# Performance work log

Measured on AMD Instinct MI355X. Metric: run time of the kernel, lower is better.

The kernel has to match this reference:

```python
import jax, jax.numpy as jnp
import numpy as np

B, S, HID = 1, 2048, 2048
N_HEADS = 16
HEAD_DIM = HID // N_HEADS  # 128
ROPE_THETA = 10000.0
NEG_INF = -1e9


def setup_inputs() -> dict:
    key = jax.random.key(0)
    ks = jax.random.split(key, 5)
    hidden_states = jax.random.normal(ks[0], (B, S, HID), dtype=jnp.float32)
    scale = 1.0 / np.sqrt(HID)
    Wq = jax.random.normal(ks[1], (HID, HID), dtype=jnp.float32) * scale
    Wk = jax.random.normal(ks[2], (HID, HID), dtype=jnp.float32) * scale
    Wv = jax.random.normal(ks[3], (HID, HID), dtype=jnp.float32) * scale
    Wo = jax.random.normal(ks[4], (HID, HID), dtype=jnp.float32) * scale
    # additive causal mask [B, 1, S, S]: 0 on/below diag, -1e9 above
    causal = jnp.tril(jnp.ones((S, S), dtype=bool))
    attention_mask = jnp.where(causal, 0.0, NEG_INF).astype(jnp.float32)[None, None]
    attention_mask = jnp.broadcast_to(attention_mask, (B, 1, S, S))
    position_ids = jnp.broadcast_to(jnp.arange(S, dtype=jnp.int64)[None, :], (B, S))
    return {"hidden_states": hidden_states, "Wq": Wq, "Wk": Wk, "Wv": Wv,
            "Wo": Wo, "attention_mask": attention_mask, "position_ids": position_ids}


def _rotate_half(x):
    x1, x2 = jnp.split(x, 2, axis=-1)
    return jnp.concatenate((-x2, x1), axis=-1)


def _rope_cos_sin(position_ids, head_dim, dtype):
    inv_freq = 1.0 / (ROPE_THETA ** (jnp.arange(0, head_dim, 2, dtype=jnp.float32) / head_dim))
    freqs = position_ids.astype(jnp.float32)[:, :, None] * inv_freq[None, None, :]  # [b, s, d/2]
    emb = jnp.concatenate((freqs, freqs), axis=-1)  # [b, s, d]
    # unsqueeze_dim=1 -> broadcast over heads
    return jnp.cos(emb).astype(dtype)[:, None], jnp.sin(emb).astype(dtype)[:, None]


def reference(hidden_states, Wq, Wk, Wv, Wo, attention_mask, position_ids):
    b, s, h = hidden_states.shape
    d = HEAD_DIM
    def proj(W):
        return (hidden_states @ W.T).reshape(b, s, N_HEADS, d).transpose(0, 2, 1, 3)  # [b,h,s,d]
    q, k, v = proj(Wq), proj(Wk), proj(Wv)
    cos, sin = _rope_cos_sin(position_ids, d, q.dtype)
    q = q * cos + _rotate_half(q) * sin
    k = k * cos + _rotate_half(k) * sin
    scores = jnp.einsum('bhqd,bhkd->bhqk', q, k) / jnp.sqrt(jnp.float32(d))
    scores = scores + attention_mask
    probs = jax.nn.softmax(scores.astype(jnp.float32), axis=-1).astype(q.dtype)
    attn = jnp.einsum('bhqk,bhkd->bhqd', probs, v)
    out = attn.transpose(0, 2, 1, 3).reshape(b, s, h)
    return out @ Wo.T
```

## Files before the change

kernel.cpp:

```cpp
#include <hip/hip_runtime.h>

typedef _Float16 half8 __attribute__((ext_vector_type(8)));
typedef _Float16 half4 __attribute__((ext_vector_type(4)));
typedef float floatx4 __attribute__((ext_vector_type(4)));
typedef float floatx16 __attribute__((ext_vector_type(16)));

#define GLDS(gp, lp) __builtin_amdgcn_global_load_lds( \
    (const __attribute__((address_space(1))) void*)(gp), \
    (__attribute__((address_space(3))) void*)(lp), 16, 0, 0)

__global__ void cvt_f2h5(const float* __restrict__ s0, const float* __restrict__ s1,
                         const float* __restrict__ s2, const float* __restrict__ s3,
                         const float* __restrict__ s4,
                         _Float16* __restrict__ d0, _Float16* __restrict__ d1,
                         _Float16* __restrict__ d2, _Float16* __restrict__ d3,
                         _Float16* __restrict__ d4, int n8) {
  int i = blockIdx.x * 256 + threadIdx.x;
  if (i >= n8) return;
  const float* s; _Float16* d;
  switch (blockIdx.y) {
    case 0: s = s0; d = d0; break;
    case 1: s = s1; d = d1; break;
    case 2: s = s2; d = d2; break;
    case 3: s = s3; d = d3; break;
    default: s = s4; d = d4; break;
  }
  const float4* s4p = (const float4*)s;
  float4 a = s4p[2 * i], b = s4p[2 * i + 1];
  half8 h;
  h[0] = (_Float16)a.x; h[1] = (_Float16)a.y; h[2] = (_Float16)a.z; h[3] = (_Float16)a.w;
  h[4] = (_Float16)b.x; h[5] = (_Float16)b.y; h[6] = (_Float16)b.z; h[7] = (_Float16)b.w;
  *(half8*)(d + 8 * (size_t)i) = h;
}

__global__ __launch_bounds__(256) void transpose_k(const _Float16* __restrict__ src,
                                                   _Float16* __restrict__ dst) {
  __shared__ _Float16 t[64][72];
  const int r0 = blockIdx.y * 64, c0 = blockIdx.x * 64;
  const int tr = threadIdx.x >> 3, tc = (threadIdx.x & 7) * 8;
  #pragma unroll
  for (int p = 0; p < 2; ++p) {
    half8 v = *(const half8*)(src + (size_t)(r0 + p * 32 + tr) * 2048 + c0 + tc);
    *(half8*)&t[p * 32 + tr][tc] = v;
  }
  __syncthreads();
  #pragma unroll
  for (int p = 0; p < 2; ++p) {
    half8 v;
    #pragma unroll
    for (int j = 0; j < 8; ++j) v[j] = t[tc + j][p * 32 + tr];
    *(half8*)(dst + (size_t)(c0 + p * 32 + tr) * 2048 + r0 + tc) = v;
  }
}

template <int OUTF, int BN>
__global__ __launch_bounds__(256) void gemm_nt(const _Float16* __restrict__ A,
                                               const _Float16* __restrict__ B,
                                               _Float16* __restrict__ Ch,
                                               float* __restrict__ Cf,
                                               long long bStride, long long cStride) {
  __shared__ _Float16 As[2][128 * 32];
  __shared__ _Float16 Bs[2][BN * 32];
  const int NF = BN / 32;
  const int tid = threadIdx.x, lane = tid & 63, wv = tid >> 6;
  const int fr = lane & 15, fg = lane >> 4;
  const int bm = blockIdx.y * 128, bn = blockIdx.x * BN;
  const _Float16* Ab = A + (size_t)bm * 2048;
  const _Float16* Bb = B + (size_t)blockIdx.z * bStride + (size_t)bn * 2048;
  const int srow = lane >> 2;
  const int scol = (lane & 3) * 8;
  const int wm = (wv >> 1) * 64, wn = (wv & 1) * (BN / 2);

  floatx4 acc[4][NF] = {};

  auto stage = [&](int buf, int kt) {
    #pragma unroll
    for (int r = 0; r < 2; ++r) {
      int row = r * 64 + wv * 16 + srow;
      GLDS(Ab + (size_t)row * 2048 + kt * 32 + scol, &As[buf][(r * 64 + wv * 16) * 32]);
    }
    #pragma unroll
    for (int r = 0; r < BN / 64; ++r) {
      int row = r * 64 + wv * 16 + srow;
      GLDS(Bb + (size_t)row * 2048 + kt * 32 + scol, &Bs[buf][(r * 64 + wv * 16) * 32]);
    }
  };

  stage(0, 0);
  __syncthreads();

  #pragma unroll 2
  for (int kt = 0; kt < 64; ++kt) {
    const int cur = kt & 1;
    if (kt < 63) stage(cur ^ 1, kt + 1);
    half8 af[4], bf[NF];
    #pragma unroll
    for (int m = 0; m < 4; ++m)
      af[m] = *(const half8*)&As[cur][(wm + m * 16 + fr) * 32 + fg * 8];
    #pragma unroll
    for (int n = 0; n < NF; ++n)
      bf[n] = *(const half8*)&Bs[cur][(wn + n * 16 + fr) * 32 + fg * 8];
    #pragma unroll
    for (int m = 0; m < 4; ++m)
      #pragma unroll
      for (int n = 0; n < NF; ++n)
        acc[m][n] = __builtin_amdgcn_mfma_f32_16x16x32_f16(af[m], bf[n], acc[m][n], 0, 0, 0);
    __syncthreads();
  }

  #pragma unroll
  for (int m = 0; m < 4; ++m)
    #pragma unroll
    for (int n = 0; n < NF; ++n)
      #pragma unroll
      for (int i = 0; i < 4; ++i) {
        const int row = bm + wm + m * 16 + fg * 4 + i;
        const int col = bn + wn + n * 16 + fr;
        if (OUTF)
          Cf[(size_t)row * 2048 + col] = acc[m][n][i];
        else
          Ch[(size_t)blockIdx.z * cStride + (size_t)row * 2048 + col] = (_Float16)acc[m][n][i];
      }
}

__global__ void rope_k(_Float16* __restrict__ Q, _Float16* __restrict__ K) {
  const int idx = blockIdx.x * 256 + threadIdx.x;
  const int s = idx >> 10;
  const int hd = idx & 1023;
  const int head = hd >> 6, d = hd & 63;
  const float freq = powf(10000.0f, -(float)d * (1.0f / 64.0f));
  const float ang = (float)s * freq;
  float sn, c;
  sincosf(ang, &sn, &c);
  const size_t base = (size_t)s * 2048 + head * 128 + d;
  float q1 = (float)Q[base], q2 = (float)Q[base + 64];
  Q[base]      = (_Float16)(q1 * c - q2 * sn);
  Q[base + 64] = (_Float16)(q2 * c + q1 * sn);
  float k1 = (float)K[base], k2 = (float)K[base + 64];
  K[base]      = (_Float16)(k1 * c - k2 * sn);
  K[base + 64] = (_Float16)(k2 * c + k1 * sn);
}

__global__ __launch_bounds__(256, 2) void attn_k(const _Float16* __restrict__ Qp,
                                                 const _Float16* __restrict__ Kp,
                                                 const _Float16* __restrict__ Vt,
                                                 _Float16* __restrict__ Op) {
  extern __shared__ _Float16 smem[];
  _Float16* Ks = smem;
  _Float16* Vs = smem + 2 * 64 * 128;
  _Float16* Pb = smem + 4 * 64 * 128;

  const int tid = threadIdx.x, lane = tid & 63, wv = tid >> 6;
  const int l31 = lane & 31, hi = lane >> 5;
  const int wq = wv >> 1, wk = wv & 1;

  const int bid = (int)blockIdx.x;
  const int halfg = bid >> 8;
  const int rr = bid & 255;
  const int xcd = rr & 7;
  const int idx = rr >> 3;
  const int head = (xcd << 1) | (idx & 1);
  const int gslot = idx >> 1;
  const int g = halfg ? gslot : 31 - gslot;
  const size_t hoff = (size_t)head * 128;
  const int q0 = g * 64;
  const int qw = q0 + wq * 32;
  _Float16* Pw = Pb + wv * (32 * 40);

  half8 qf[8];
  const _Float16 scl = (_Float16)0.08838834764831845f;
  #pragma unroll
  for (int ks = 0; ks < 8; ++ks) {
    half8 t = *(const half8*)(Qp + (size_t)(qw + l31) * 2048 + hoff + ks * 16 + hi * 8);
    #pragma unroll
    for (int j = 0; j < 8; ++j) t[j] = (_Float16)(t[j] * scl);
    qf[ks] = t;
  }

  auto stage = [&](int buf, int it) {
    const int kv0 = it * 64;
    #pragma unroll
    for (int i = 0; i < 4; ++i) {
      const int rbase = wv * 16 + i * 4;
      const int row = rbase + (lane >> 4);
      const int gr = (lane & 15) ^ (row & 7);
      GLDS(Kp + (size_t)(kv0 + row) * 2048 + hoff + gr * 8,
           Ks + buf * 8192 + rbase * 128);
    }
    #pragma unroll
    for (int i = 0; i < 4; ++i) {
      const int rbase = wv * 32 + i * 8;
      const int row = rbase + (lane >> 3);
      const int gr = (lane & 7) ^ (row & 7);
      GLDS(Vt + (size_t)(hoff + row) * 2048 + kv0 + gr * 8,
           Vs + buf * 8192 + rbase * 64);
    }
  };

  floatx16 o[4] = {};
  float rsum = 0.0f;

  stage(0, 0);
  __syncthreads();

  int buf = 0;
  for (int it = 0; it <= g; ++it) {
    if (it < g) stage(buf ^ 1, it + 1);
    const _Float16* Kb = Ks + buf * 8192;
    const _Float16* Vb = Vs + buf * 8192;

    const int krow = wk * 32 + l31;
    const int ksw = l31 & 7;
    floatx16 S = {};
    __builtin_amdgcn_s_setprio(1);
    #pragma unroll
    for (int ks = 0; ks < 8; ++ks) {
      half8 a = *(const half8*)(Kb + krow * 128 + (((ks * 2 + hi) ^ ksw) * 8));
      S = __builtin_amdgcn_mfma_f32_32x32x16_f16(a, qf[ks], S, 0, 0, 0);
    }
    __builtin_amdgcn_s_setprio(0);

    if (it == g) {
      const int kv0 = it * 64;
      const int qa = qw + l31;
      #pragma unroll
      for (int r = 0; r < 16; ++r) {
        const int ka = kv0 + wk * 32 + (r & 3) + 8 * (r >> 2) + 4 * hi;
        if (ka > qa) S[r] = -1e30f;
      }
    }

    #pragma unroll
    for (int r4 = 0; r4 < 4; ++r4) {
      float p0 = __expf(S[4 * r4 + 0] - 8.0f);
      float p1 = __expf(S[4 * r4 + 1] - 8.0f);
      float p2 = __expf(S[4 * r4 + 2] - 8.0f);
      float p3 = __expf(S[4 * r4 + 3] - 8.0f);
      rsum += (p0 + p1) + (p2 + p3);
      half4 pk;
      pk[0] = (_Float16)p0; pk[1] = (_Float16)p1;
      pk[2] = (_Float16)p2; pk[3] = (_Float16)p3;
      *(half4*)(Pw + l31 * 40 + r4 * 8 + hi * 4) = pk;
    }

    half8 pa0 = *(const half8*)(Pw + l31 * 40 + hi * 8);
    half8 pa1 = *(const half8*)(Pw + l31 * 40 + 16 + hi * 8);

    __builtin_amdgcn_s_setprio(1);
    #pragma unroll
    for (int dt = 0; dt < 4; ++dt) {
      const int vrow = dt * 32 + l31;
      const int vsw = vrow & 7;
      half8 b0 = *(const half8*)(Vb + vrow * 64 + (((wk * 4 + hi) ^ vsw) * 8));
      half8 b1 = *(const half8*)(Vb + vrow * 64 + (((wk * 4 + 2 + hi) ^ vsw) * 8));
      o[dt] = __builtin_amdgcn_mfma_f32_32x32x16_f16(pa0, b0, o[dt], 0, 0, 0);
      o[dt] = __builtin_amdgcn_mfma_f32_32x32x16_f16(pa1, b1, o[dt], 0, 0, 0);
    }
    __builtin_amdgcn_s_setprio(0);

    __syncthreads();
    buf ^= 1;
  }

  float* Mo = (float*)smem;
  float* Mr = (float*)(smem + 16384);
  if (wk == 1) {
    #pragma unroll
    for (int dt = 0; dt < 4; ++dt)
      #pragma unroll
      for (int r = 0; r < 16; ++r)
        Mo[((wq * 4 + dt) * 16 + r) * 64 + lane] = o[dt][r];
    Mr[wq * 64 + lane] = rsum;
  }
  __syncthreads();
  if (wk == 0) {
    rsum += Mr[wq * 64 + lane];
    float rs = rsum;
    rs += __shfl_xor(rs, 32);
    const float inv = 1.0f / rs;
    float invq[16];
    #pragma unroll
    for (int r = 0; r < 16; ++r)
      invq[r] = __shfl(inv, (r & 3) + 8 * (r >> 2) + 4 * hi);
    #pragma unroll
    for (int dt = 0; dt < 4; ++dt)
      #pragma unroll
      for (int r = 0; r < 16; ++r) {
        const float w = (o[dt][r] + Mo[((wq * 4 + dt) * 16 + r) * 64 + lane]) * invq[r];
        const int qa = qw + (r & 3) + 8 * (r >> 2) + 4 * hi;
        Op[(size_t)qa * 2048 + hoff + dt * 32 + l31] = (_Float16)w;
      }
  }
}

extern "C" void kernel_launch(void* const* d_in, const int* in_sizes, int n_in,
                              void* d_out, int out_size, void* d_ws, size_t ws_size,
                              hipStream_t stream) {
  (void)in_sizes; (void)n_in; (void)out_size; (void)ws_size;
  const float* X  = (const float*)d_in[0];
  const float* Wq = (const float*)d_in[1];
  const float* Wk = (const float*)d_in[2];
  const float* Wv = (const float*)d_in[3];
  const float* Wo = (const float*)d_in[4];
  float* out = (float*)d_out;

  const size_t SZ = 2048ull * 2048ull;
  _Float16* ws  = (_Float16*)d_ws;
  _Float16* Xh  = ws + 0 * SZ;
  _Float16* Wqh = ws + 1 * SZ;
  _Float16* Wkh = ws + 2 * SZ;
  _Float16* Wvh = ws + 3 * SZ;
  _Float16* Woh = ws + 4 * SZ;
  _Float16* Qp  = ws + 5 * SZ;
  _Float16* Kp  = ws + 6 * SZ;
  _Float16* Vp  = ws + 7 * SZ;
  _Float16* Vtg = Wqh;
  _Float16* At  = Xh;

  const int n8 = (int)(SZ / 8);
  dim3 blk(256);

  cvt_f2h5<<<dim3(n8 / 256, 5), blk, 0, stream>>>(X, Wq, Wk, Wv, Wo,
                                                  Xh, Wqh, Wkh, Wvh, Woh, n8);

  gemm_nt<0, 128><<<dim3(16, 16, 3), blk, 0, stream>>>(Xh, Wqh, Qp, nullptr,
                                                       (long long)SZ, (long long)SZ);
  rope_k<<<(2048 * 1024) / 256, blk, 0, stream>>>(Qp, Kp);
  transpose_k<<<dim3(32, 32), blk, 0, stream>>>(Vp, Vtg);

  const size_t attn_lds = (4 * 64 * 128 + 4 * 32 * 40) * sizeof(_Float16);
  attn_k<<<512, blk, attn_lds, stream>>>(Qp, Kp, Vtg, At);

  gemm_nt<1, 64><<<dim3(32, 16, 1), blk, 0, stream>>>(At, Woh, nullptr, out, 0, 0);
}
```

Measured before the change: 178.0 us.

## Split long causal attention rows across two blocks and merge; swizzle GEMM LDS

Query tiles in the upper half of the causal range are now split at KV tile 16 into two work units, so the attention grid grows to 768 roughly balanced blocks. Each block writes an unnormalised partial output and a row sum to workspace, and a new merge kernel adds the partials and normalises them. Separately, the GEMM staging and fragment reads use an XOR swizzle on the 8-element column chunk to cut LDS bank conflicts. The split relies on the softmax having no running-max rescaling, so plain addition of partials is valid. It costs an extra kernel launch and a round trip of the partials through global memory.

```diff
diff --git a/kernel.cpp b/kernel.cpp
--- a/kernel.cpp
+++ b/kernel.cpp
@@ -68,8 +68,8 @@
   const _Float16* Ab = A + (size_t)bm * 2048;
   const _Float16* Bb = B + (size_t)blockIdx.z * bStride + (size_t)bn * 2048;
   const int srow = lane >> 2;
-  const int scol = (lane & 3) * 8;
-  const int wm = (wv >> 1) * 64, wn = (wv & 1) * (BN / 2);
+  const int gsw = (lane & 3) ^ ((lane >> 3) & 3);
+  const int asw = (fr >> 1) & 3;
 
   floatx4 acc[4][NF] = {};
 
@@ -77,14 +77,15 @@
     #pragma unroll
     for (int r = 0; r < 2; ++r) {
       int row = r * 64 + wv * 16 + srow;
-      GLDS(Ab + (size_t)row * 2048 + kt * 32 + scol, &As[buf][(r * 64 + wv * 16) * 32]);
+      GLDS(Ab + (size_t)row * 2048 + kt * 32 + gsw * 8, &As[buf][(r * 64 + wv * 16) * 32]);
     }
     #pragma unroll
     for (int r = 0; r < BN / 64; ++r) {
       int row = r * 64 + wv * 16 + srow;
-      GLDS(Bb + (size_t)row * 2048 + kt * 32 + scol, &Bs[buf][(r * 64 + wv * 16) * 32]);
+      GLDS(Bb + (size_t)row * 2048 + kt * 32 + gsw * 8, &Bs[buf][(r * 64 + wv * 16) * 32]);
     }
   };
+  const int wm = (wv >> 1) * 64, wn = (wv & 1) * (BN / 2);
 
   stage(0, 0);
   __syncthreads();
@@ -96,10 +97,10 @@
     half8 af[4], bf[NF];
     #pragma unroll
     for (int m = 0; m < 4; ++m)
-      af[m] = *(const half8*)&As[cur][(wm + m * 16 + fr) * 32 + fg * 8];
+      af[m] = *(const half8*)&As[cur][(wm + m * 16 + fr) * 32 + ((fg ^ asw) * 8)];
     #pragma unroll
     for (int n = 0; n < NF; ++n)
-      bf[n] = *(const half8*)&Bs[cur][(wn + n * 16 + fr) * 32 + fg * 8];
+      bf[n] = *(const half8*)&Bs[cur][(wn + n * 16 + fr) * 32 + ((fg ^ asw) * 8)];
     #pragma unroll
     for (int m = 0; m < 4; ++m)
       #pragma unroll
@@ -144,7 +145,8 @@
 __global__ __launch_bounds__(256, 2) void attn_k(const _Float16* __restrict__ Qp,
                                                  const _Float16* __restrict__ Kp,
                                                  const _Float16* __restrict__ Vt,
-                                                 _Float16* __restrict__ Op) {
+                                                 _Float16* __restrict__ Po,
+                                                 float* __restrict__ Pr) {
   extern __shared__ _Float16 smem[];
   _Float16* Ks = smem;
   _Float16* Vs = smem + 2 * 64 * 128;
@@ -155,16 +157,17 @@
   const int wq = wv >> 1, wk = wv & 1;
 
   const int bid = (int)blockIdx.x;
-  const int halfg = bid >> 8;
-  const int rr = bid & 255;
-  const int xcd = rr & 7;
-  const int idx = rr >> 3;
-  const int head = (xcd << 1) | (idx & 1);
-  const int gslot = idx >> 1;
-  const int g = halfg ? gslot : 31 - gslot;
+  const int head = ((bid & 7) << 1) | ((bid >> 3) & 1);
+  const int L = bid >> 4;
+  int g, it0, itEnd;
+  if (L < 16) { g = 16 + L; it0 = 0; itEnd = 16; }
+  else {
+    const int j = (L - 16) >> 1;
+    if ((L & 1) == 0) { g = 15 - j; it0 = 0; itEnd = g + 1; }
+    else             { g = 31 - j; it0 = 16; itEnd = g + 1; }
+  }
   const size_t hoff = (size_t)head * 128;
-  const int q0 = g * 64;
-  const int qw = q0 + wq * 32;
+  const int qw = g * 64 + wq * 32;
   _Float16* Pw = Pb + wv * (32 * 40);
 
   half8 qf[8];
@@ -200,12 +203,12 @@
   floatx16 o[4] = {};
   float rsum = 0.0f;
 
-  stage(0, 0);
+  stage(0, it0);
   __syncthreads();
 
   int buf = 0;
-  for (int it = 0; it <= g; ++it) {
-    if (it < g) stage(buf ^ 1, it + 1);
+  for (int it = it0; it < itEnd; ++it) {
+    if (it + 1 < itEnd) stage(buf ^ 1, it + 1);
     const _Float16* Kb = Ks + buf * 8192;
     const _Float16* Vb = Vs + buf * 8192;
 
@@ -277,19 +280,48 @@
     rsum += Mr[wq * 64 + lane];
     float rs = rsum;
     rs += __shfl_xor(rs, 32);
-    const float inv = 1.0f / rs;
-    float invq[16];
-    #pragma unroll
-    for (int r = 0; r < 16; ++r)
-      invq[r] = __shfl(inv, (r & 3) + 8 * (r >> 2) + 4 * hi);
+    if (hi == 0) Pr[(size_t)bid * 64 + wq * 32 + l31] = rs;
     #pragma unroll
     for (int dt = 0; dt < 4; ++dt)
       #pragma unroll
       for (int r = 0; r < 16; ++r) {
-        const float w = (o[dt][r] + Mo[((wq * 4 + dt) * 16 + r) * 64 + lane]) * invq[r];
-        const int qa = qw + (r & 3) + 8 * (r >> 2) + 4 * hi;
-        Op[(size_t)qa * 2048 + hoff + dt * 32 + l31] = (_Float16)w;
+        const float w = o[dt][r] + Mo[((wq * 4 + dt) * 16 + r) * 64 + lane];
+        const int ql = wq * 32 + (r & 3) + 8 * (r >> 2) + 4 * hi;
+        Po[(size_t)bid * 8192 + ql * 128 + dt * 32 + l31] = (_Float16)w;
       }
+  }
+}
+
+__global__ __launch_bounds__(256) void attn_merge(const _Float16* __restrict__ Po,
+                                                  const float* __restrict__ Pr,
+                                                  _Float16* __restrict__ At) {
+  const int bidx = (int)blockIdx.x;
+  const int h = bidx & 15, g = bidx >> 4;
+  const int hb = ((h & 1) << 3) | (h >> 1);
+  const int L0 = (g >= 16) ? (g - 16) : (16 + 2 * (15 - g));
+  const int U0 = L0 * 16 + hb;
+  const bool two = (g >= 16);
+  const int U1 = two ? ((17 + 2 * (31 - g)) * 16 + hb) : 0;
+  const int t = threadIdx.x;
+  const int q = t >> 2, cs = t & 3;
+  const float r0 = Pr[(size_t)U0 * 64 + q];
+  const float r1 = two ? Pr[(size_t)U1 * 64 + q] : 0.0f;
+  const float inv = 1.0f / (r0 + r1);
+  const size_t orow = (size_t)(g * 64 + q) * 2048 + h * 128;
+  #pragma unroll
+  for (int s = 0; s < 4; ++s) {
+    const int d0 = (cs + s * 4) * 8;
+    half8 a = *(const half8*)(Po + (size_t)U0 * 8192 + q * 128 + d0);
+    half8 o;
+    if (two) {
+      half8 b = *(const half8*)(Po + (size_t)U1 * 8192 + q * 128 + d0);
+      #pragma unroll
+      for (int j = 0; j < 8; ++j) o[j] = (_Float16)(((float)a[j] + (float)b[j]) * inv);
+    } else {
+      #pragma unroll
+      for (int j = 0; j < 8; ++j) o[j] = (_Float16)((float)a[j] * inv);
+    }
+    *(half8*)(At + orow + d0) = o;
   }
 }
 
@@ -316,6 +348,8 @@
   _Float16* Vp  = ws + 7 * SZ;
   _Float16* Vtg = Wqh;
   _Float16* At  = Xh;
+  _Float16* Po  = Wkh;
+  float*    Pr  = (float*)Vp;
 
   const int n8 = (int)(SZ / 8);
   dim3 blk(256);
@@ -329,7 +363,8 @@
   transpose_k<<<dim3(32, 32), blk, 0, stream>>>(Vp, Vtg);
 
   const size_t attn_lds = (4 * 64 * 128 + 4 * 32 * 40) * sizeof(_Float16);
-  attn_k<<<512, blk, attn_lds, stream>>>(Qp, Kp, Vtg, At);
+  attn_k<<<768, blk, attn_lds, stream>>>(Qp, Kp, Vtg, Po, Pr);
+  attn_merge<<<512, blk, 0, stream>>>(Po, Pr, At);
 
   gemm_nt<1, 64><<<dim3(32, 16, 1), blk, 0, stream>>>(At, Woh, nullptr, out, 0, 0);
 }
```

After: 179.9 us. No clear change (+1.0%).
